# Performance work log

Hardware: AMD Instinct MI355X
Metric: run time of the kernel (lower is better)

The kernel has to match this reference:

```python
import jax, jax.numpy as jnp
import numpy as np

B, H, S, D = 2, 16, 2048, 128


def setup_inputs() -> dict:
    key = jax.random.key(0)
    kq, kk, kv, km, kb = jax.random.split(key, 5)
    q = jax.random.normal(kq, (B, H, S, D), dtype=jnp.float32)
    k = jax.random.normal(kk, (B, H, S, D), dtype=jnp.float32)
    v = jax.random.normal(kv, (B, H, S, D), dtype=jnp.float32)
    mask = jax.random.randint(km, (B, 1, S, S), 0, 2, dtype=jnp.int32)
    rel_bias = jax.random.normal(kb, (H, S, S), dtype=jnp.float32)
    return {"q": q, "k": k, "v": v, "mask": mask, "rel_bias": rel_bias}


def reference(q, k, v, mask, rel_bias):
    d_k = q.shape[-1]
    scale = 1.0 / jnp.sqrt(jnp.float32(d_k)).astype(q.dtype)
    # scores: [B,H,S,S]
    scores = jnp.einsum("bhqd,bhkd->bhqk", q, k) * scale
    scores = scores + rel_bias[None, :, :, :]  # broadcast batch
    NEG = jnp.asarray(-1e9, dtype=scores.dtype)
    scores = jnp.where(mask == 0, NEG, scores)
    attn = jax.nn.softmax(scores, axis=-1)
    # dropout p=0.0 -> identity (reference uses eval/deterministic dropout)
    out = jnp.einsum("bhqk,bhkd->bhqd", attn, v)
    return (out, attn)
```

## Files before the change

kernel.cpp:

```cpp
#include <hip/hip_runtime.h>

#define B_ 2
#define H_ 16
#define S_ 2048
#define D_ 128

typedef __attribute__((ext_vector_type(8))) short short8;
typedef __attribute__((ext_vector_type(4))) float floatx4;

__device__ __forceinline__ unsigned short f2bf(float f) {
    union { float f; unsigned int u; } c; c.f = f;
    unsigned int u = c.u;
    u += 0x7fff + ((u >> 16) & 1);
    return (unsigned short)(u >> 16);
}

__device__ __forceinline__ void gld16(const void* g, void* l) {
    __builtin_amdgcn_global_load_lds(
        (const __attribute__((address_space(1))) unsigned int*)(unsigned long long)g,
        (__attribute__((address_space(3))) unsigned int*)(unsigned int)(unsigned long long)l,
        16, 0, 0);
}

__global__ __launch_bounds__(256) void kbf_kernel(const float* __restrict__ k,
                                                  unsigned short* __restrict__ kw) {
    int base = blockIdx.x * 1024 + threadIdx.x;
    #pragma unroll
    for (int i = 0; i < 4; ++i) {
        int idx = base + i * 256;
        const float4* s = (const float4*)k + (size_t)idx * 2;
        float4 a = s[0], c = s[1];
        short8 y;
        y[0] = f2bf(a.x); y[1] = f2bf(a.y); y[2] = f2bf(a.z); y[3] = f2bf(a.w);
        y[4] = f2bf(c.x); y[5] = f2bf(c.y); y[6] = f2bf(c.z); y[7] = f2bf(c.w);
        ((short8*)kw)[idx] = y;
    }
}

__global__ __launch_bounds__(256) void vt_kernel(const float* __restrict__ v,
                                                 unsigned short* __restrict__ vt) {
    __shared__ unsigned short tl[128][66];
    int bid = blockIdx.x;
    int bh = bid >> 5;
    int s0 = (bid & 31) << 6;
    int t = threadIdx.x;
    const float4* vp = (const float4*)(v + ((size_t)bh * S_ + s0) * D_);
    #pragma unroll
    for (int i = 0; i < 8; ++i) {
        int idx = t + i * 256;
        int r = idx >> 5;
        int d = (idx & 31) << 2;
        float4 x = vp[idx];
        tl[d + 0][r] = f2bf(x.x);
        tl[d + 1][r] = f2bf(x.y);
        tl[d + 2][r] = f2bf(x.z);
        tl[d + 3][r] = f2bf(x.w);
    }
    __syncthreads();
    unsigned short* op = vt + (size_t)bh * D_ * S_ + s0;
    #pragma unroll
    for (int i = 0; i < 16; ++i) {
        int idx = t + i * 256;
        int d = idx >> 5;
        int s2 = (idx & 31) << 1;
        unsigned int val = (unsigned int)tl[d][s2] | ((unsigned int)tl[d][s2 + 1] << 16);
        *(unsigned int*)(op + (size_t)d * S_ + s2) = val;
    }
}


#define LOAD_BM(BB, MM, K0) do {                                              \
    _Pragma("unroll") for (int rr = 0; rr < 4; ++rr) {                        \
        _Pragma("unroll") for (int nt = 0; nt < 4; ++nt) {                    \
            BB[rr * 4 + nt] = bias_r[rr][(K0) + nt * 16];                     \
            MM[rr * 4 + nt] = mask_r[rr][(K0) + nt * 16]; } } } while (0)

#define QK_MFMA(KB, ACC) do {                                                 \
    _Pragma("unroll") for (int nt = 0; nt < 4; ++nt)                          \
        ACC[nt] = (floatx4){0.f, 0.f, 0.f, 0.f};                              \
    _Pragma("unroll") for (int kk = 0; kk < 4; ++kk) {                        \
        _Pragma("unroll") for (int nt = 0; nt < 4; ++nt) {                    \
            int r_ = nt * 16 + l16;                                           \
            short8 bfr_ = *(const short8*)((const char*)(KB) + r_ * 256 +     \
                           ((kk * 64 + g * 16) ^ ((r_ & 7) << 4)));           \
            ACC[nt] = __builtin_amdgcn_mfma_f32_16x16x32_bf16(                \
                          afr[kk], bfr_, ACC[nt], 0, 0, 0); } } } while (0)

#define ERS(BB, MM) do {                                                      \
    _Pragma("unroll") for (int rr = 0; rr < 4; ++rr) {                        \
        _Pragma("unroll") for (int nt = 0; nt < 4; ++nt) {                    \
            float e_ = MM[rr * 4 + nt]                                        \
                ? __expf(fmaf(acc[nt][rr], scale, BB[rr * 4 + nt])) : 0.f;    \
            rs[rr] += e_; } } } while (0)

__global__ __launch_bounds__(256, 3) void attn_kernel(
    const float* __restrict__ q,
    const int* __restrict__ mask,
    const float* __restrict__ bias,
    const unsigned short* __restrict__ ktw,
    const unsigned short* __restrict__ vtw,
    float* __restrict__ attn,
    float* __restrict__ out)
{
    __shared__ __align__(16) char smem[40960];
    unsigned short* kbuf0 = (unsigned short*)smem;
    unsigned short* kbuf1 = (unsigned short*)(smem + 16384);
    unsigned short* pbuf  = (unsigned short*)(smem + 32768);

    int bid = blockIdx.x;
    int qt = bid >> 5;
    int hb = bid & 31;
    int h = hb >> 1;
    int b = hb & 1;
    int bh = b * H_ + h;
    int q0 = qt << 6;
    int t = threadIdx.x;
    int w = t >> 6;
    int lane = t & 63;
    int g = lane >> 4;
    int l16 = lane & 15;

    const unsigned short* ktw_bh = ktw + (size_t)bh * S_ * D_;
    const unsigned short* vtw_bh = vtw + (size_t)bh * D_ * S_;

    short8 afr[4];
    {
        const float* qrow = q + ((size_t)bh * S_ + q0 + w * 16 + l16) * D_;
        #pragma unroll
        for (int kk = 0; kk < 4; ++kk) {
            float4 a = *(const float4*)&qrow[kk * 32 + g * 8];
            float4 c = *(const float4*)&qrow[kk * 32 + g * 8 + 4];
            short8 f;
            f[0] = f2bf(a.x); f[1] = f2bf(a.y); f[2] = f2bf(a.z); f[3] = f2bf(a.w);
            f[4] = f2bf(c.x); f[5] = f2bf(c.y); f[6] = f2bf(c.z); f[7] = f2bf(c.w);
            afr[kk] = f;
        }
    }

    const float* bias_r[4];
    const int*   mask_r[4];
    {
        const float* bh_bias = bias + (size_t)h * S_ * S_;
        const int*   b_mask  = mask + (size_t)b * S_ * S_;
        #pragma unroll
        for (int rr = 0; rr < 4; ++rr) {
            int row = q0 + w * 16 + g * 4 + rr;
            bias_r[rr] = bh_bias + (size_t)row * S_ + l16;
            mask_r[rr] = b_mask  + (size_t)row * S_ + l16;
        }
    }

    auto stage_k = [&](int k0, unsigned short* kb) {
        int rsub = lane >> 4;
        int cb = (lane & 15) << 4;
        #pragma unroll
        for (int c = 0; c < 4; ++c) {
            int r = w * 16 + c * 4 + rsub;
            const char* src = (const char*)ktw_bh + (((size_t)(k0 + r)) << 8)
                              + (cb ^ ((r & 7) << 4));
            gld16(src, (char*)kb + w * 4096 + c * 1024);
        }
    };
    auto stage_v = [&](int k0) {
        int dsub = lane >> 3;
        int cb = (lane & 7) << 4;
        #pragma unroll
        for (int c = 0; c < 4; ++c) {
            int d = w * 32 + c * 8 + dsub;
            const char* src = (const char*)vtw_bh + (size_t)d * (S_ * 2)
                              + (size_t)(k0 * 2) + (cb ^ ((d & 7) << 4));
            gld16(src, (char*)kbuf1 + w * 4096 + c * 1024);
        }
    };

    const float scale = 0.08838834764831845f;
    float rs[4] = {0.f, 0.f, 0.f, 0.f};
    float bbA[16], bbB[16];
    int   mmA[16], mmB[16];

    stage_k(0, kbuf0);
    LOAD_BM(bbA, mmA, 0);
    __syncthreads();

    #pragma unroll 1
    for (int ktp = 0; ktp < 16; ++ktp) {
        int kt0 = ktp << 1;
        stage_k((kt0 + 1) << 6, kbuf1);
        LOAD_BM(bbB, mmB, (kt0 + 1) << 6);
        {
            floatx4 acc[4];
            QK_MFMA(kbuf0, acc);
            ERS(bbA, mmA);
        }
        __syncthreads();
        if (kt0 < 30) {
            stage_k((kt0 + 2) << 6, kbuf0);
            LOAD_BM(bbA, mmA, (kt0 + 2) << 6);
        }
        {
            floatx4 acc[4];
            QK_MFMA(kbuf1, acc);
            ERS(bbB, mmB);
        }
        __syncthreads();
    }

    float rinv[4];
    #pragma unroll
    for (int rr = 0; rr < 4; ++rr) {
        float s = rs[rr];
        s += __shfl_xor(s, 1, 16);
        s += __shfl_xor(s, 2, 16);
        s += __shfl_xor(s, 4, 16);
        s += __shfl_xor(s, 8, 16);
        rinv[rr] = s > 0.f ? 1.0f / s : 0.f;
    }

    floatx4 oacc[8];
    #pragma unroll
    for (int nt = 0; nt < 8; ++nt) oacc[nt] = (floatx4){0.f, 0.f, 0.f, 0.f};

    stage_k(0, kbuf0);
    stage_v(0);
    LOAD_BM(bbA, mmA, 0);
    __syncthreads();

    float* attn_r = attn + (size_t)bh * S_ * S_
                  + (size_t)(q0 + w * 16 + g * 4) * S_ + l16;

    #pragma unroll 1
    for (int kt = 0; kt < 32; ++kt) {
        int k0 = kt << 6;
        floatx4 acc[4];
        QK_MFMA(kbuf0, acc);

        float p[16];
        #pragma unroll
        for (int rr = 0; rr < 4; ++rr) {
            #pragma unroll
            for (int nt = 0; nt < 4; ++nt) {
                float e_ = mmA[rr * 4 + nt]
                    ? __expf(fmaf(acc[nt][rr], scale, bbA[rr * 4 + nt])) : 0.f;
                float pv_ = e_ * rinv[rr];
                p[rr * 4 + nt] = pv_;
                int prow = g * 4 + rr;
                *(unsigned short*)((char*)pbuf + (w << 11) + prow * 128 +
                    ((nt * 32 + (l16 << 1)) ^ ((prow & 7) << 4))) = f2bf(pv_);
            }
        }
        if (kt < 31) LOAD_BM(bbA, mmA, k0 + 64);

        #pragma unroll
        for (int kk = 0; kk < 2; ++kk) {
            short8 pa = *(const short8*)((const char*)pbuf + (w << 11) +
                          l16 * 128 + ((kk * 64 + g * 16) ^ ((l16 & 7) << 4)));
            #pragma unroll
            for (int nt = 0; nt < 8; ++nt) {
                int d_ = nt * 16 + l16;
                short8 vf = *(const short8*)((const char*)kbuf1 + d_ * 128 +
                              ((kk * 64 + g * 16) ^ ((d_ & 7) << 4)));
                oacc[nt] = __builtin_amdgcn_mfma_f32_16x16x32_bf16(pa, vf, oacc[nt], 0, 0, 0);
            }
        }
        __syncthreads();
        if (kt < 31) { stage_k(k0 + 64, kbuf0); stage_v(k0 + 64); }
        #pragma unroll
        for (int rr = 0; rr < 4; ++rr)
            #pragma unroll
            for (int nt = 0; nt < 4; ++nt)
                attn_r[rr * S_ + k0 + nt * 16] = p[rr * 4 + nt];
        __syncthreads();
    }

    float* op = out + ((size_t)bh * S_ + q0 + w * 16 + g * 4) * D_ + l16;
    #pragma unroll
    for (int nt = 0; nt < 8; ++nt)
        #pragma unroll
        for (int rr = 0; rr < 4; ++rr)
            op[(size_t)rr * D_ + nt * 16] = oacc[nt][rr];
}

extern "C" void kernel_launch(void* const* d_in, const int* in_sizes, int n_in,
                              void* d_out, int out_size, void* d_ws, size_t ws_size,
                              hipStream_t stream) {
    (void)in_sizes; (void)n_in; (void)out_size; (void)ws_size;
    const float* q    = (const float*)d_in[0];
    const float* k    = (const float*)d_in[1];
    const float* v    = (const float*)d_in[2];
    const int*   mask = (const int*)d_in[3];
    const float* bias = (const float*)d_in[4];

    float* out  = (float*)d_out;
    float* attn = out + (size_t)B_ * H_ * S_ * D_;

    unsigned short* ktw = (unsigned short*)d_ws;
    unsigned short* vtw = ktw + (size_t)B_ * H_ * S_ * D_;

    kbf_kernel<<<1024, 256, 0, stream>>>(k, ktw);
    vt_kernel<<<1024, 256, 0, stream>>>(v, vtw);
    attn_kernel<<<1024, 256, 0, stream>>>(q, mask, bias, ktw, vtw, attn, out);
}
```

Before: 1.156 ms.

## Load K/V MFMA fragments directly from global, drop LDS staging and barriers

Removes the shared-memory staging of K and V tiles, which used async global-to-LDS copies and block-wide barriers, and has each lane read its bf16 MFMA operand fragments straight from global memory. LDS drops to a small per-wave P buffer, so no __syncthreads is needed and occupancy can rise. The mask is also folded into the bias as -1e30 at load time, which removes the select in the exp path, and the second pass is unrolled two key tiles per iteration. The cost is that each wave of a block now re-reads K and V fragments from global memory or L2 with less coalesced access, instead of sharing one LDS copy per block.

Measured after the change: 1.820 ms. +57.5%, slower.

```diff
diff --git a/kernel.cpp b/kernel.cpp
--- a/kernel.cpp
+++ b/kernel.cpp
@@ -13,13 +13,6 @@
     unsigned int u = c.u;
     u += 0x7fff + ((u >> 16) & 1);
     return (unsigned short)(u >> 16);
-}
-
-__device__ __forceinline__ void gld16(const void* g, void* l) {
-    __builtin_amdgcn_global_load_lds(
-        (const __attribute__((address_space(1))) unsigned int*)(unsigned long long)g,
-        (__attribute__((address_space(3))) unsigned int*)(unsigned int)(unsigned long long)l,
-        16, 0, 0);
 }
 
 __global__ __launch_bounds__(256) void kbf_kernel(const float* __restrict__ k,
@@ -69,29 +62,49 @@
 }
 
 
-#define LOAD_BM(BB, MM, K0) do {                                              \
+#define LOAD_BM(BB, K0) do {                                                  \
     _Pragma("unroll") for (int rr = 0; rr < 4; ++rr) {                        \
         _Pragma("unroll") for (int nt = 0; nt < 4; ++nt) {                    \
-            BB[rr * 4 + nt] = bias_r[rr][(K0) + nt * 16];                     \
-            MM[rr * 4 + nt] = mask_r[rr][(K0) + nt * 16]; } } } while (0)
-
-#define QK_MFMA(KB, ACC) do {                                                 \
+            int m_ = mask_r[rr][(K0) + nt * 16];                              \
+            float bv_ = bias_r[rr][(K0) + nt * 16];                           \
+            BB[rr * 4 + nt] = m_ ? bv_ : -1e30f; } } } while (0)
+
+#define QK_MFMA(K0, ACC) do {                                                 \
     _Pragma("unroll") for (int nt = 0; nt < 4; ++nt)                          \
         ACC[nt] = (floatx4){0.f, 0.f, 0.f, 0.f};                              \
     _Pragma("unroll") for (int kk = 0; kk < 4; ++kk) {                        \
         _Pragma("unroll") for (int nt = 0; nt < 4; ++nt) {                    \
-            int r_ = nt * 16 + l16;                                           \
-            short8 bfr_ = *(const short8*)((const char*)(KB) + r_ * 256 +     \
-                           ((kk * 64 + g * 16) ^ ((r_ & 7) << 4)));           \
+            short8 bfr_ = *(const short8*)(kfrag + (K0) * 256 +               \
+                                           nt * 4096 + kk * 64);              \
             ACC[nt] = __builtin_amdgcn_mfma_f32_16x16x32_bf16(                \
                           afr[kk], bfr_, ACC[nt], 0, 0, 0); } } } while (0)
 
-#define ERS(BB, MM) do {                                                      \
+#define ERS(BB) do {                                                          \
     _Pragma("unroll") for (int rr = 0; rr < 4; ++rr) {                        \
         _Pragma("unroll") for (int nt = 0; nt < 4; ++nt) {                    \
-            float e_ = MM[rr * 4 + nt]                                        \
-                ? __expf(fmaf(acc[nt][rr], scale, BB[rr * 4 + nt])) : 0.f;    \
-            rs[rr] += e_; } } } while (0)
+            rs[rr] += __expf(fmaf(acc[nt][rr], scale, BB[rr * 4 + nt]));      \
+        } } } while (0)
+
+#define STEP(K0, BB) do {                                                     \
+    floatx4 acc[4];                                                           \
+    QK_MFMA(K0, acc);                                                         \
+    _Pragma("unroll") for (int rr = 0; rr < 4; ++rr) {                        \
+        _Pragma("unroll") for (int nt = 0; nt < 4; ++nt) {                    \
+            float pv_ = __expf(fmaf(acc[nt][rr], scale, BB[rr * 4 + nt]))     \
+                        * rinv[rr];                                           \
+            attn_r[rr * S_ + (K0) + nt * 16] = pv_;                           \
+            int prow_ = g * 4 + rr;                                           \
+            *(unsigned short*)(pbase + prow_ * 128 +                          \
+                ((nt * 32 + (l16 << 1)) ^ ((prow_ & 7) << 4))) = f2bf(pv_);   \
+        } }                                                                   \
+    _Pragma("unroll") for (int kk = 0; kk < 2; ++kk) {                        \
+        short8 pa_ = *(const short8*)(pbase + l16 * 128 +                     \
+                        ((kk * 64 + g * 16) ^ ((l16 & 7) << 4)));             \
+        _Pragma("unroll") for (int nt = 0; nt < 8; ++nt) {                    \
+            short8 vf_ = *(const short8*)(vfrag + nt * 65536 +                \
+                                          (K0) * 2 + kk * 64);                \
+            oacc[nt] = __builtin_amdgcn_mfma_f32_16x16x32_bf16(               \
+                           pa_, vf_, oacc[nt], 0, 0, 0); } } } while (0)
 
 __global__ __launch_bounds__(256, 3) void attn_kernel(
     const float* __restrict__ q,
@@ -102,10 +115,7 @@
     float* __restrict__ attn,
     float* __restrict__ out)
 {
-    __shared__ __align__(16) char smem[40960];
-    unsigned short* kbuf0 = (unsigned short*)smem;
-    unsigned short* kbuf1 = (unsigned short*)(smem + 16384);
-    unsigned short* pbuf  = (unsigned short*)(smem + 32768);
+    __shared__ __align__(16) char smem[8192];
 
     int bid = blockIdx.x;
     int qt = bid >> 5;
@@ -120,8 +130,11 @@
     int g = lane >> 4;
     int l16 = lane & 15;
 
-    const unsigned short* ktw_bh = ktw + (size_t)bh * S_ * D_;
-    const unsigned short* vtw_bh = vtw + (size_t)bh * D_ * S_;
+    const char* kfrag = (const char*)(ktw + (size_t)bh * S_ * D_)
+                        + l16 * 256 + g * 16;
+    const char* vfrag = (const char*)(vtw + (size_t)bh * D_ * S_)
+                        + l16 * 4096 + g * 16;
+    char* pbase = smem + (w << 11);
 
     short8 afr[4];
     {
@@ -150,59 +163,26 @@
         }
     }
 
-    auto stage_k = [&](int k0, unsigned short* kb) {
-        int rsub = lane >> 4;
-        int cb = (lane & 15) << 4;
-        #pragma unroll
-        for (int c = 0; c < 4; ++c) {
-            int r = w * 16 + c * 4 + rsub;
-            const char* src = (const char*)ktw_bh + (((size_t)(k0 + r)) << 8)
-                              + (cb ^ ((r & 7) << 4));
-            gld16(src, (char*)kb + w * 4096 + c * 1024);
-        }
-    };
-    auto stage_v = [&](int k0) {
-        int dsub = lane >> 3;
-        int cb = (lane & 7) << 4;
-        #pragma unroll
-        for (int c = 0; c < 4; ++c) {
-            int d = w * 32 + c * 8 + dsub;
-            const char* src = (const char*)vtw_bh + (size_t)d * (S_ * 2)
-                              + (size_t)(k0 * 2) + (cb ^ ((d & 7) << 4));
-            gld16(src, (char*)kbuf1 + w * 4096 + c * 1024);
-        }
-    };
-
     const float scale = 0.08838834764831845f;
     float rs[4] = {0.f, 0.f, 0.f, 0.f};
     float bbA[16], bbB[16];
-    int   mmA[16], mmB[16];
-
-    stage_k(0, kbuf0);
-    LOAD_BM(bbA, mmA, 0);
-    __syncthreads();
-
+
+    LOAD_BM(bbA, 0);
     #pragma unroll 1
     for (int ktp = 0; ktp < 16; ++ktp) {
-        int kt0 = ktp << 1;
-        stage_k((kt0 + 1) << 6, kbuf1);
-        LOAD_BM(bbB, mmB, (kt0 + 1) << 6);
+        int k0 = ktp << 7;
+        LOAD_BM(bbB, k0 + 64);
         {
             floatx4 acc[4];
-            QK_MFMA(kbuf0, acc);
-            ERS(bbA, mmA);
-        }
-        __syncthreads();
-        if (kt0 < 30) {
-            stage_k((kt0 + 2) << 6, kbuf0);
-            LOAD_BM(bbA, mmA, (kt0 + 2) << 6);
-        }
+            QK_MFMA(k0, acc);
+            ERS(bbA);
+        }
+        if (ktp < 15) LOAD_BM(bbA, k0 + 128);
         {
             floatx4 acc[4];
-            QK_MFMA(kbuf1, acc);
-            ERS(bbB, mmB);
-        }
-        __syncthreads();
+            QK_MFMA(k0 + 64, acc);
+            ERS(bbB);
+        }
     }
 
     float rinv[4];
@@ -220,56 +200,17 @@
     #pragma unroll
     for (int nt = 0; nt < 8; ++nt) oacc[nt] = (floatx4){0.f, 0.f, 0.f, 0.f};
 
-    stage_k(0, kbuf0);
-    stage_v(0);
-    LOAD_BM(bbA, mmA, 0);
-    __syncthreads();
-
     float* attn_r = attn + (size_t)bh * S_ * S_
                   + (size_t)(q0 + w * 16 + g * 4) * S_ + l16;
 
+    LOAD_BM(bbA, 0);
     #pragma unroll 1
-    for (int kt = 0; kt < 32; ++kt) {
-        int k0 = kt << 6;
-        floatx4 acc[4];
-        QK_MFMA(kbuf0, acc);
-
-        float p[16];
-        #pragma unroll
-        for (int rr = 0; rr < 4; ++rr) {
-            #pragma unroll
-            for (int nt = 0; nt < 4; ++nt) {
-                float e_ = mmA[rr * 4 + nt]
-                    ? __expf(fmaf(acc[nt][rr], scale, bbA[rr * 4 + nt])) : 0.f;
-                float pv_ = e_ * rinv[rr];
-                p[rr * 4 + nt] = pv_;
-                int prow = g * 4 + rr;
-                *(unsigned short*)((char*)pbuf + (w << 11) + prow * 128 +
-                    ((nt * 32 + (l16 << 1)) ^ ((prow & 7) << 4))) = f2bf(pv_);
-            }
-        }
-        if (kt < 31) LOAD_BM(bbA, mmA, k0 + 64);
-
-        #pragma unroll
-        for (int kk = 0; kk < 2; ++kk) {
-            short8 pa = *(const short8*)((const char*)pbuf + (w << 11) +
-                          l16 * 128 + ((kk * 64 + g * 16) ^ ((l16 & 7) << 4)));
-            #pragma unroll
-            for (int nt = 0; nt < 8; ++nt) {
-                int d_ = nt * 16 + l16;
-                short8 vf = *(const short8*)((const char*)kbuf1 + d_ * 128 +
-                              ((kk * 64 + g * 16) ^ ((d_ & 7) << 4)));
-                oacc[nt] = __builtin_amdgcn_mfma_f32_16x16x32_bf16(pa, vf, oacc[nt], 0, 0, 0);
-            }
-        }
-        __syncthreads();
-        if (kt < 31) { stage_k(k0 + 64, kbuf0); stage_v(k0 + 64); }
-        #pragma unroll
-        for (int rr = 0; rr < 4; ++rr)
-            #pragma unroll
-            for (int nt = 0; nt < 4; ++nt)
-                attn_r[rr * S_ + k0 + nt * 16] = p[rr * 4 + nt];
-        __syncthreads();
+    for (int ktp = 0; ktp < 16; ++ktp) {
+        int k0 = ktp << 7;
+        LOAD_BM(bbB, k0 + 64);
+        STEP(k0, bbA);
+        if (ktp < 15) LOAD_BM(bbA, k0 + 128);
+        STEP(k0 + 64, bbB);
     }
 
     float* op = out + ((size_t)bh * S_ + q0 + w * 16 + g * 4) * D_ + l16;
```
